# Kernel tuning notes

Hardware: AMD Instinct MI355X
Metric: run time of the kernel (lower is better)

Reference implementation:

```python
import jax, jax.numpy as jnp
import numpy as np

NEG_SLOPE = 0.2

def leaky_relu(x):
    return jnp.where(x >= 0, x, NEG_SLOPE * x)

def conv1x1(x, w, b):
    # x: [n,c,h,w], w: [o,c], b: [o]
    return jnp.einsum('nchw,oc->nohw', x, w) + b[None, :, None, None]

def setup_inputs() -> dict:
    key = jax.random.key(0)
    ks = jax.random.split(key, 7)
    n, c, h, w = 4, 64, 80, 80
    scale = 1.0 / np.sqrt(c)
    return {
        'x': jax.random.normal(ks[0], (n, c, h, w), dtype=jnp.float32),
        'w1': jax.random.normal(ks[1], (c, c), dtype=jnp.float32) * scale,
        'b1': jax.random.normal(ks[2], (c,), dtype=jnp.float32) * 0.01,
        'w2': jax.random.normal(ks[3], (c, c), dtype=jnp.float32) * scale,
        'b2': jax.random.normal(ks[4], (c,), dtype=jnp.float32) * 0.01,
        'w3': jax.random.normal(ks[5], (c, c), dtype=jnp.float32) * scale,
        'b3': jax.random.normal(ks[6], (c,), dtype=jnp.float32) * 0.01,
    }

def reference(x, w1, b1, w2, b2, w3, b3):
    n, c, h, w = x.shape
    e1 = leaky_relu(conv1x1(x, w1, b1))  # [n,c,h,w]
    e2 = leaky_relu(conv1x1(x, w2, b2))
    asm = leaky_relu(conv1x1(x, w3, b3))
    # q: [n, hw, c]; k: [n, c, hw]
    q = e1.transpose(0, 2, 3, 1).reshape(n, h * w, c)
    k = e2.reshape(n, c, h * w)
    score = jax.nn.softmax(jnp.matmul(q, k), axis=2)  # [n, hw, hw]
    v = asm.reshape(n, c, h * w).transpose(0, 2, 1)   # [n, hw, c]
    out = jnp.matmul(score, v)                        # [n, hw, c]
    return out.transpose(0, 2, 1).reshape(n, c, h, w)
```

## Files before the change

### kernel.cpp

```cpp
#include <hip/hip_runtime.h>


typedef __attribute__((ext_vector_type(8))) unsigned short us8;
typedef __attribute__((ext_vector_type(4))) unsigned short us4;
typedef __attribute__((ext_vector_type(8))) __bf16 bf16x8;
typedef __attribute__((ext_vector_type(16))) float f32x16;

#define HW 6400
#define L2E 1.44269504088896340736f
#define KS 5
#define ITERS 20

union V8 { us8 s; us4 h[2]; bf16x8 b; unsigned u4[4]; };

__device__ __forceinline__ unsigned short f32_to_bf16(float f) {
  unsigned u = __float_as_uint(f);
  u += 0x7fffu + ((u >> 16) & 1u);
  return (unsigned short)(u >> 16);
}
__device__ __forceinline__ float bf16_bits_to_f32(unsigned short u) {
  return __uint_as_float(((unsigned)u) << 16);
}
__device__ __forceinline__ unsigned pack_bf16x2(float a, float b) {
#if __has_builtin(__builtin_amdgcn_cvt_pk_bf16_f32)
  auto v = __builtin_amdgcn_cvt_pk_bf16_f32(a, b);
  unsigned u;
  __builtin_memcpy(&u, &v, 4);
  return u;
#else
  unsigned ua = __float_as_uint(a); ua += 0x7fffu + ((ua >> 16) & 1u);
  unsigned ub = __float_as_uint(b); ub += 0x7fffu + ((ub >> 16) & 1u);
  return (ua >> 16) | (ub & 0xffff0000u);
#endif
}

__device__ __forceinline__ void split_hilo(const float* f, V8& hi, V8& lo) {
#pragma unroll
  for (int j = 0; j < 8; ++j) {
    const unsigned short h = f32_to_bf16(f[j]);
    const float r = f[j] - bf16_bits_to_f32(h);
    hi.s[j] = h;
    lo.s[j] = f32_to_bf16(r);
  }
}

__global__ __launch_bounds__(256, 2) void conv_kernel(
    const float* __restrict__ x,
    const float* __restrict__ w1, const float* __restrict__ b1,
    const float* __restrict__ w2, const float* __restrict__ b2,
    const float* __restrict__ w3, const float* __restrict__ b3,
    unsigned short* __restrict__ Qg, unsigned short* __restrict__ Kg,
    unsigned short* __restrict__ Vg) {
  __shared__ __align__(16) float xs[64 * 132];
  __shared__ __align__(16) unsigned short tb[128 * 72];

  const int t = threadIdx.x;
  const int n = blockIdx.y;
  const int p0 = blockIdx.x * 128;
  const int k = blockIdx.z;
  const int wv = t >> 6;
  const int lane = t & 63;
  const int l31 = lane & 31;
  const int lh = lane >> 5;
  const int ob = (wv & 1) * 32;
  const int pw = (wv >> 1) * 64;

  {
    const int c = t >> 2, qq = t & 3;
    const float* src = x + ((size_t)(n * 64 + c) * HW + p0 + qq * 32);
    float* dst = xs + c * 132 + qq * 32;
#pragma unroll
    for (int i = 0; i < 8; ++i)
      *(float4*)(dst + i * 4) = *(const float4*)(src + i * 4);
  }
  __syncthreads();

  const float* wm = (k == 0) ? w1 : (k == 1) ? w2 : w3;
  const float* bm = (k == 0) ? b1 : (k == 1) ? b2 : b3;

  V8 ah[4], al[4];
#pragma unroll
  for (int kst = 0; kst < 4; ++kst) {
    const float* wr = wm + (size_t)(ob + l31) * 64 + kst * 16 + lh * 8;
    float wf[8];
    *(float4*)(wf) = *(const float4*)wr;
    *(float4*)(wf + 4) = *(const float4*)(wr + 4);
    split_hilo(wf, ah[kst], al[kst]);
  }

  f32x16 acc[2];
#pragma unroll
  for (int pb = 0; pb < 2; ++pb)
#pragma unroll
    for (int r = 0; r < 16; ++r) acc[pb][r] = 0.f;

#pragma unroll
  for (int kst = 0; kst < 4; ++kst) {
#pragma unroll
    for (int pb = 0; pb < 2; ++pb) {
      float xf[8];
      const float* xp = xs + (kst * 16 + lh * 8) * 132 + pw + pb * 32 + l31;
#pragma unroll
      for (int j = 0; j < 8; ++j) xf[j] = xp[j * 132];
      V8 bh, bl;
      split_hilo(xf, bh, bl);
      acc[pb] = __builtin_amdgcn_mfma_f32_32x32x16_bf16(al[kst].b, bh.b, acc[pb], 0, 0, 0);
      acc[pb] = __builtin_amdgcn_mfma_f32_32x32x16_bf16(ah[kst].b, bl.b, acc[pb], 0, 0, 0);
      acc[pb] = __builtin_amdgcn_mfma_f32_32x32x16_bf16(ah[kst].b, bh.b, acc[pb], 0, 0, 0);
    }
  }

  if (k < 2) {
#pragma unroll
    for (int pb = 0; pb < 2; ++pb) {
#pragma unroll
      for (int rq = 0; rq < 4; ++rq) {
        const int o = ob + 8 * rq + 4 * lh;
        const int pcol = pw + pb * 32 + l31;
        float v[4];
#pragma unroll
        for (int j = 0; j < 4; ++j) {
          float a = acc[pb][4 * rq + j] + bm[o + j];
          a = fmaxf(a, 0.f) + 0.2f * fminf(a, 0.f);
          if (k == 0) a *= L2E;
          v[j] = a;
        }
        unsigned* dst = (unsigned*)(tb + pcol * 72 + o);
        dst[0] = pack_bf16x2(v[0], v[1]);
        dst[1] = pack_bf16x2(v[2], v[3]);
      }
    }
    __syncthreads();
    {
      const int p = t >> 1, half = t & 1;
      const unsigned short* src = tb + p * 72 + half * 32;
      unsigned short* dst = (k == 0 ? Qg : Kg) +
                            (size_t)(n * HW + p0 + p) * 64 + half * 32;
#pragma unroll
      for (int i = 0; i < 4; ++i) *(us8*)(dst + i * 8) = *(const us8*)(src + i * 8);
    }
  } else {
#pragma unroll
    for (int pb = 0; pb < 2; ++pb) {
#pragma unroll
      for (int r = 0; r < 16; ++r) {
        const int o = ob + 8 * (r >> 2) + 4 * lh + (r & 3);
        const int pcol = pw + pb * 32 + l31;
        float a = acc[pb][r] + bm[o];
        a = fmaxf(a, 0.f) + 0.2f * fminf(a, 0.f);
        Vg[(size_t)(n * 64 + o) * HW + p0 + pcol] = f32_to_bf16(a);
      }
    }
  }
}

__global__ __launch_bounds__(256, 4) void attn_kernel(
    const unsigned short* __restrict__ Qg, const unsigned short* __restrict__ Kg,
    const unsigned short* __restrict__ Vg, unsigned short* __restrict__ Opart,
    float* __restrict__ Lpart) {
  __shared__ __align__(16) char smem[36864];
  unsigned short* Otb = (unsigned short*)smem;

  const int t = threadIdx.x;
  const int w = t >> 6;
  const int lane = t & 63;
  const int l31 = lane & 31;
  const int lh = lane >> 5;
  const int nb = blockIdx.y;
  const int qb = blockIdx.x * 128;
  const int ks = blockIdx.z;
  const int key0 = ks * (HW / KS);

  V8 aQ[4];
  {
    const unsigned short* qrow =
        Qg + (size_t)(nb * HW + qb + w * 32 + l31) * 64 + lh * 8;
#pragma unroll
    for (int kst = 0; kst < 4; ++kst) aQ[kst].s = *(const us8*)(qrow + kst * 16);
  }

  f32x16 accO[2];
#pragma unroll
  for (int ci = 0; ci < 2; ++ci)
#pragma unroll
    for (int r = 0; r < 16; ++r) accO[ci][r] = 0.f;
  float lp = 0.f;

  f32x16 zero16;
#pragma unroll
  for (int r = 0; r < 16; ++r) zero16[r] = 0.f;

  const int soff = (t >> 2) * 72 + (t & 3) * 16;
  const unsigned short* ksrc =
      Kg + (size_t)nb * HW * 64 + (size_t)(key0 + (t >> 2)) * 64 + (t & 3) * 16;
  const unsigned short* vsrc =
      Vg + (size_t)nb * 64 * HW + (size_t)(t >> 2) * HW + key0 + (t & 3) * 16;

  V8 kr0, kr1, vr0, vr1;
  kr0.s = *(const us8*)ksrc;
  kr1.s = *(const us8*)(ksrc + 8);
  vr0.s = *(const us8*)vsrc;
  vr1.s = *(const us8*)(vsrc + 8);
  {
    unsigned short* kd = (unsigned short*)smem + soff;
    unsigned short* vd = (unsigned short*)(smem + 18432) + soff;
    *(us8*)kd = kr0.s; *(us8*)(kd + 8) = kr1.s;
    *(us8*)vd = vr0.s; *(us8*)(vd + 8) = vr1.s;
  }
  __syncthreads();

#pragma unroll 1
  for (int jt = 0; jt < ITERS; ++jt) {
    const int b = jt & 1;
    const unsigned short* Kc = (const unsigned short*)(smem + b * 9216);
    const unsigned short* Vc = (const unsigned short*)(smem + 18432 + b * 9216);
    const bool more = (jt + 1 < ITERS);

    if (more) {
      kr0.s = *(const us8*)(ksrc + (jt + 1) * 4096);
      kr1.s = *(const us8*)(ksrc + (jt + 1) * 4096 + 8);
      vr0.s = *(const us8*)(vsrc + (jt + 1) * 64);
      vr1.s = *(const us8*)(vsrc + (jt + 1) * 64 + 8);
    }

#pragma unroll
    for (int ni = 0; ni < 2; ++ni) {
      V8 ak[4];
#pragma unroll
      for (int kst = 0; kst < 4; ++kst)
        ak[kst].s = *(const us8*)(Kc + (ni * 32 + l31) * 72 + kst * 16 + lh * 8);
      f32x16 sacc =
          __builtin_amdgcn_mfma_f32_32x32x16_bf16(ak[0].b, aQ[0].b, zero16, 0, 0, 0);
#pragma unroll
      for (int kst = 1; kst < 4; ++kst)
        sacc = __builtin_amdgcn_mfma_f32_32x32x16_bf16(ak[kst].b, aQ[kst].b,
                                                       sacc, 0, 0, 0);
      uint2 pkg[4];
#pragma unroll
      for (int g = 0; g < 4; ++g) {
        const float p0 = __builtin_amdgcn_exp2f(sacc[4 * g + 0]);
        const float p1 = __builtin_amdgcn_exp2f(sacc[4 * g + 1]);
        const float p2 = __builtin_amdgcn_exp2f(sacc[4 * g + 2]);
        const float p3 = __builtin_amdgcn_exp2f(sacc[4 * g + 3]);
        lp += (p0 + p1) + (p2 + p3);
        pkg[g].x = pack_bf16x2(p0, p1);
        pkg[g].y = pack_bf16x2(p2, p3);
      }

      V8 bv[2][2];
#pragma unroll
      for (int ci = 0; ci < 2; ++ci)
#pragma unroll
        for (int kk = 0; kk < 2; ++kk)
          bv[ci][kk].s = *(const us8*)(Vc + (ci * 32 + l31) * 72 +
                                       (2 * ni + kk) * 16 + lh * 8);
#pragma unroll
      for (int kk = 0; kk < 2; ++kk) {
        const int gb = 2 * kk;
        V8 ap;
#if __has_builtin(__builtin_amdgcn_permlane32_swap)
        {
          auto rx = __builtin_amdgcn_permlane32_swap(pkg[gb].x, pkg[gb + 1].x,
                                                     false, false);
          auto ry = __builtin_amdgcn_permlane32_swap(pkg[gb].y, pkg[gb + 1].y,
                                                     false, false);
          ap.u4[0] = rx[0]; ap.u4[2] = rx[1];
          ap.u4[1] = ry[0]; ap.u4[3] = ry[1];
        }
#else
        {
          const uint2 qa = pkg[gb];
          const uint2 qb2 = pkg[gb + 1];
          uint2 send;
          send.x = lh ? qa.x : qb2.x;
          send.y = lh ? qa.y : qb2.y;
          uint2 recv;
          recv.x = __shfl_xor(send.x, 32);
          recv.y = __shfl_xor(send.y, 32);
          const uint2 keep = {lh ? qb2.x : qa.x, lh ? qb2.y : qa.y};
          ap.u4[0] = lh ? recv.x : keep.x;
          ap.u4[1] = lh ? recv.y : keep.y;
          ap.u4[2] = lh ? keep.x : recv.x;
          ap.u4[3] = lh ? keep.y : recv.y;
        }
#endif
        accO[0] = __builtin_amdgcn_mfma_f32_32x32x16_bf16(ap.b, bv[0][kk].b,
                                                          accO[0], 0, 0, 0);
        accO[1] = __builtin_amdgcn_mfma_f32_32x32x16_bf16(ap.b, bv[1][kk].b,
                                                          accO[1], 0, 0, 0);
      }
    }

    if (more) {
      unsigned short* kd = (unsigned short*)(smem + (1 - b) * 9216) + soff;
      unsigned short* vd = (unsigned short*)(smem + 18432 + (1 - b) * 9216) + soff;
      *(us8*)kd = kr0.s; *(us8*)(kd + 8) = kr1.s;
      *(us8*)vd = vr0.s; *(us8*)(vd + 8) = vr1.s;
      __syncthreads();
    }
  }

  {
    const float lsum = lp + __shfl_xor(lp, 32);
    if (lh == 0)
      Lpart[((size_t)ks * 4 + nb) * HW + qb + w * 32 + l31] = lsum;
  }

  __syncthreads();
#pragma unroll
  for (int ci = 0; ci < 2; ++ci)
#pragma unroll
    for (int r = 0; r < 16; ++r) {
      const int qcol = w * 32 + 8 * (r >> 2) + 4 * lh + (r & 3);
      Otb[(ci * 32 + l31) * 132 + qcol] = f32_to_bf16(accO[ci][r]);
    }
  __syncthreads();
  {
    const int ch = t >> 2, part = t & 3;
    const unsigned short* src = Otb + ch * 132 + part * 32;
    unsigned short* dst =
        Opart + (((size_t)ks * 4 + nb) * 64 + ch) * HW + qb + part * 32;
#pragma unroll
    for (int i = 0; i < 4; ++i) {
      V8 v;
      v.h[0] = *(const us4*)(src + i * 8);
      v.h[1] = *(const us4*)(src + i * 8 + 4);
      *(us8*)(dst + i * 8) = v.s;
    }
  }
}

__global__ __launch_bounds__(256) void combine_kernel(
    const unsigned short* __restrict__ Opart, const float* __restrict__ Lpart,
    float* __restrict__ out) {
  const int tid = blockIdx.x * 256 + threadIdx.x;
  const size_t e = (size_t)tid * 4;
  float4 o = {0.f, 0.f, 0.f, 0.f};
#pragma unroll
  for (int ks = 0; ks < KS; ++ks) {
    const us4 v = *(const us4*)(Opart + (size_t)ks * (4 * 64 * HW) + e);
    o.x += bf16_bits_to_f32(v[0]);
    o.y += bf16_bits_to_f32(v[1]);
    o.z += bf16_bits_to_f32(v[2]);
    o.w += bf16_bits_to_f32(v[3]);
  }
  const int n = (int)(e / (64 * HW));
  const int p = (int)(e % HW);
  float4 l = {0.f, 0.f, 0.f, 0.f};
#pragma unroll
  for (int ks = 0; ks < KS; ++ks) {
    const float4 v = *(const float4*)(Lpart + ((size_t)ks * 4 + n) * HW + p);
    l.x += v.x; l.y += v.y; l.z += v.z; l.w += v.w;
  }
  float4 r;
  r.x = o.x / l.x; r.y = o.y / l.y; r.z = o.z / l.z; r.w = o.w / l.w;
  *(float4*)(out + e) = r;
}

extern "C" void kernel_launch(void* const* d_in, const int* in_sizes, int n_in,
                              void* d_out, int out_size, void* d_ws, size_t ws_size,
                              hipStream_t stream) {
  const float* x = (const float*)d_in[0];
  const float* w1 = (const float*)d_in[1];
  const float* b1 = (const float*)d_in[2];
  const float* w2 = (const float*)d_in[3];
  const float* b2 = (const float*)d_in[4];
  const float* w3 = (const float*)d_in[5];
  const float* b3 = (const float*)d_in[6];
  float* out = (float*)d_out;

  unsigned short* Q = (unsigned short*)d_ws;
  unsigned short* K = Q + (size_t)4 * HW * 64;
  unsigned short* V = K + (size_t)4 * HW * 64;
  unsigned short* Opart = V + (size_t)4 * HW * 64;
  float* Lpart = (float*)(Opart + (size_t)KS * 4 * 64 * HW);

  conv_kernel<<<dim3(50, 4, 3), 256, 0, stream>>>(x, w1, b1, w2, b2, w3, b3,
                                                  Q, K, V);
  attn_kernel<<<dim3(50, 4, KS), 256, 0, stream>>>(Q, K, V, Opart, Lpart);
  combine_kernel<<<1600, 256, 0, stream>>>(Opart, Lpart, out);
}
```

Baseline: 145.2 us.

## Precompute split weights and compute all three projections per block from shared x

A small prep kernel splits the weights into bf16 hi/lo pairs once, folds the log2(e) scale into w1 and b1, and writes them to workspace. The conv kernel now loads each 64-pixel x tile once, converts it to hi/lo bf16 in shared memory, and loops over the three projections, so x is no longer read and split three times. This cuts redundant global reads and conversion work. In exchange it adds an extra kernel launch, halves the pixel tile (100 blocks instead of 150), and runs the three projections serially inside each block.

```diff
diff --git a/kernel.cpp b/kernel.cpp
--- a/kernel.cpp
+++ b/kernel.cpp
@@ -34,119 +34,128 @@
 #endif
 }
 
-__device__ __forceinline__ void split_hilo(const float* f, V8& hi, V8& lo) {
-#pragma unroll
-  for (int j = 0; j < 8; ++j) {
-    const unsigned short h = f32_to_bf16(f[j]);
-    const float r = f[j] - bf16_bits_to_f32(h);
-    hi.s[j] = h;
-    lo.s[j] = f32_to_bf16(r);
-  }
+__global__ __launch_bounds__(256) void wprep_kernel(
+    const float* __restrict__ w1, const float* __restrict__ b1,
+    const float* __restrict__ w2, const float* __restrict__ w3,
+    unsigned short* __restrict__ Whl, float* __restrict__ b1s) {
+  const int tid = blockIdx.x * 256 + threadIdx.x;
+  if (tid < 3 * 4096) {
+    const int k = tid >> 12;
+    const int rem = tid & 4095;
+    const float* wsrc = (k == 0) ? w1 : (k == 1) ? w2 : w3;
+    float v = wsrc[rem];
+    if (k == 0) v *= L2E;
+    const unsigned short hi = f32_to_bf16(v);
+    const unsigned short lo = f32_to_bf16(v - bf16_bits_to_f32(hi));
+    Whl[(size_t)(k * 2) * 4096 + rem] = hi;
+    Whl[(size_t)(k * 2 + 1) * 4096 + rem] = lo;
+  }
+  if (tid < 64) b1s[tid] = b1[tid] * L2E;
 }
 
 __global__ __launch_bounds__(256, 2) void conv_kernel(
-    const float* __restrict__ x,
-    const float* __restrict__ w1, const float* __restrict__ b1,
-    const float* __restrict__ w2, const float* __restrict__ b2,
-    const float* __restrict__ w3, const float* __restrict__ b3,
+    const float* __restrict__ x, const unsigned short* __restrict__ Whl,
+    const float* __restrict__ b1s, const float* __restrict__ b2,
+    const float* __restrict__ b3,
     unsigned short* __restrict__ Qg, unsigned short* __restrict__ Kg,
     unsigned short* __restrict__ Vg) {
-  __shared__ __align__(16) float xs[64 * 132];
-  __shared__ __align__(16) unsigned short tb[128 * 72];
+  __shared__ __align__(16) unsigned short Xh[64 * 72];
+  __shared__ __align__(16) unsigned short Xl[64 * 72];
+  __shared__ __align__(16) unsigned short tb[64 * 72];
 
   const int t = threadIdx.x;
   const int n = blockIdx.y;
-  const int p0 = blockIdx.x * 128;
-  const int k = blockIdx.z;
+  const int p0 = blockIdx.x * 64;
   const int wv = t >> 6;
   const int lane = t & 63;
   const int l31 = lane & 31;
   const int lh = lane >> 5;
   const int ob = (wv & 1) * 32;
-  const int pw = (wv >> 1) * 64;
-
-  {
-    const int c = t >> 2, qq = t & 3;
-    const float* src = x + ((size_t)(n * 64 + c) * HW + p0 + qq * 32);
-    float* dst = xs + c * 132 + qq * 32;
-#pragma unroll
-    for (int i = 0; i < 8; ++i)
-      *(float4*)(dst + i * 4) = *(const float4*)(src + i * 4);
+  const int pw = (wv >> 1) * 32;
+
+  {
+    const int c2 = t >> 3;
+    const int pg = (t & 7) * 8;
+    const float* s0 = x + ((size_t)(n * 64 + 2 * c2) * HW + p0 + pg);
+    const float* s1 = s0 + HW;
+    float a0[8], a1[8];
+    *(float4*)(a0) = *(const float4*)s0;
+    *(float4*)(a0 + 4) = *(const float4*)(s0 + 4);
+    *(float4*)(a1) = *(const float4*)s1;
+    *(float4*)(a1 + 4) = *(const float4*)(s1 + 4);
+#pragma unroll
+    for (int j = 0; j < 8; ++j) {
+      const unsigned hp = pack_bf16x2(a0[j], a1[j]);
+      const float r0 = a0[j] - bf16_bits_to_f32((unsigned short)(hp & 0xffffu));
+      const float r1 = a1[j] - bf16_bits_to_f32((unsigned short)(hp >> 16));
+      const unsigned lq = pack_bf16x2(r0, r1);
+      ((unsigned*)Xh)[(pg + j) * 36 + c2] = hp;
+      ((unsigned*)Xl)[(pg + j) * 36 + c2] = lq;
+    }
   }
   __syncthreads();
 
-  const float* wm = (k == 0) ? w1 : (k == 1) ? w2 : w3;
-  const float* bm = (k == 0) ? b1 : (k == 1) ? b2 : b3;
-
-  V8 ah[4], al[4];
-#pragma unroll
-  for (int kst = 0; kst < 4; ++kst) {
-    const float* wr = wm + (size_t)(ob + l31) * 64 + kst * 16 + lh * 8;
-    float wf[8];
-    *(float4*)(wf) = *(const float4*)wr;
-    *(float4*)(wf + 4) = *(const float4*)(wr + 4);
-    split_hilo(wf, ah[kst], al[kst]);
-  }
-
-  f32x16 acc[2];
-#pragma unroll
-  for (int pb = 0; pb < 2; ++pb)
-#pragma unroll
-    for (int r = 0; r < 16; ++r) acc[pb][r] = 0.f;
-
-#pragma unroll
-  for (int kst = 0; kst < 4; ++kst) {
-#pragma unroll
-    for (int pb = 0; pb < 2; ++pb) {
-      float xf[8];
-      const float* xp = xs + (kst * 16 + lh * 8) * 132 + pw + pb * 32 + l31;
-#pragma unroll
-      for (int j = 0; j < 8; ++j) xf[j] = xp[j * 132];
+#pragma unroll 1
+  for (int k = 0; k < 3; ++k) {
+    const unsigned short* Wh = Whl + (size_t)(k * 2) * 4096;
+    const unsigned short* Wl = Wh + 4096;
+    const float* bm = (k == 0) ? b1s : (k == 1) ? b2 : b3;
+
+    V8 ah[4], al[4];
+#pragma unroll
+    for (int kst = 0; kst < 4; ++kst) {
+      const int off = (ob + l31) * 64 + kst * 16 + lh * 8;
+      ah[kst].s = *(const us8*)(Wh + off);
+      al[kst].s = *(const us8*)(Wl + off);
+    }
+
+    f32x16 acc;
+#pragma unroll
+    for (int r = 0; r < 16; ++r) acc[r] = 0.f;
+
+#pragma unroll
+    for (int kst = 0; kst < 4; ++kst) {
       V8 bh, bl;
-      split_hilo(xf, bh, bl);
-      acc[pb] = __builtin_amdgcn_mfma_f32_32x32x16_bf16(al[kst].b, bh.b, acc[pb], 0, 0, 0);
-      acc[pb] = __builtin_amdgcn_mfma_f32_32x32x16_bf16(ah[kst].b, bl.b, acc[pb], 0, 0, 0);
-      acc[pb] = __builtin_amdgcn_mfma_f32_32x32x16_bf16(ah[kst].b, bh.b, acc[pb], 0, 0, 0);
-    }
-  }
-
-  if (k < 2) {
-#pragma unroll
-    for (int pb = 0; pb < 2; ++pb) {
+      const int xoff = (pw + l31) * 72 + kst * 16 + lh * 8;
+      bh.s = *(const us8*)(Xh + xoff);
+      bl.s = *(const us8*)(Xl + xoff);
+      acc = __builtin_amdgcn_mfma_f32_32x32x16_bf16(al[kst].b, bh.b, acc, 0, 0, 0);
+      acc = __builtin_amdgcn_mfma_f32_32x32x16_bf16(ah[kst].b, bl.b, acc, 0, 0, 0);
+      acc = __builtin_amdgcn_mfma_f32_32x32x16_bf16(ah[kst].b, bh.b, acc, 0, 0, 0);
+    }
+
+    if (k < 2) {
 #pragma unroll
       for (int rq = 0; rq < 4; ++rq) {
         const int o = ob + 8 * rq + 4 * lh;
-        const int pcol = pw + pb * 32 + l31;
+        const int pcol = pw + l31;
         float v[4];
 #pragma unroll
         for (int j = 0; j < 4; ++j) {
-          float a = acc[pb][4 * rq + j] + bm[o + j];
+          float a = acc[4 * rq + j] + bm[o + j];
           a = fmaxf(a, 0.f) + 0.2f * fminf(a, 0.f);
-          if (k == 0) a *= L2E;
           v[j] = a;
         }
         unsigned* dst = (unsigned*)(tb + pcol * 72 + o);
         dst[0] = pack_bf16x2(v[0], v[1]);
         dst[1] = pack_bf16x2(v[2], v[3]);
       }
-    }
-    __syncthreads();
-    {
-      const int p = t >> 1, half = t & 1;
-      const unsigned short* src = tb + p * 72 + half * 32;
-      unsigned short* dst = (k == 0 ? Qg : Kg) +
-                            (size_t)(n * HW + p0 + p) * 64 + half * 32;
-#pragma unroll
-      for (int i = 0; i < 4; ++i) *(us8*)(dst + i * 8) = *(const us8*)(src + i * 8);
-    }
-  } else {
-#pragma unroll
-    for (int pb = 0; pb < 2; ++pb) {
+      __syncthreads();
+      {
+        const int p = t >> 2, part = t & 3;
+        const unsigned short* src = tb + p * 72 + part * 16;
+        unsigned short* dst = (k == 0 ? Qg : Kg) +
+                              (size_t)(n * HW + p0 + p) * 64 + part * 16;
+        *(us8*)dst = *(const us8*)src;
+        *(us8*)(dst + 8) = *(const us8*)(src + 8);
+      }
+      __syncthreads();
+    } else {
 #pragma unroll
       for (int r = 0; r < 16; ++r) {
         const int o = ob + 8 * (r >> 2) + 4 * lh + (r & 3);
-        const int pcol = pw + pb * 32 + l31;
-        float a = acc[pb][r] + bm[o];
+        const int pcol = pw + l31;
+        float a = acc[r] + bm[o];
         a = fmaxf(a, 0.f) + 0.2f * fminf(a, 0.f);
         Vg[(size_t)(n * 64 + o) * HW + p0 + pcol] = f32_to_bf16(a);
       }
@@ -374,9 +383,11 @@
   unsigned short* V = K + (size_t)4 * HW * 64;
   unsigned short* Opart = V + (size_t)4 * HW * 64;
   float* Lpart = (float*)(Opart + (size_t)KS * 4 * 64 * HW);
-
-  conv_kernel<<<dim3(50, 4, 3), 256, 0, stream>>>(x, w1, b1, w2, b2, w3, b3,
-                                                  Q, K, V);
+  unsigned short* Whl = (unsigned short*)(Lpart + (size_t)KS * 4 * HW);
+  float* b1s = (float*)(Whl + 3 * 2 * 4096);
+
+  wprep_kernel<<<48, 256, 0, stream>>>(w1, b1, w2, w3, Whl, b1s);
+  conv_kernel<<<dim3(100, 4), 256, 0, stream>>>(x, Whl, b1s, b2, b3, Q, K, V);
   attn_kernel<<<dim3(50, 4, KS), 256, 0, stream>>>(Q, K, V, Opart, Lpart);
   combine_kernel<<<1600, 256, 0, stream>>>(Opart, Lpart, out);
 }
```

New measurement: 145.3 us. About the same (+0.1%).
